# Performance work log

Measured on AMD Instinct MI355X. Metric: run time of the kernel, lower is better.

The kernel has to match this reference:

```python
import jax, jax.numpy as jnp
import numpy as np

B, BOUNDS, NRIM, K, UNITS = 4096, 512, 6, 4, 600
H_IN, DK_IN, DV_IN = 4, 64, 400
H_C, DK_C, DV_C = 4, 32, 100


def setup_inputs() -> dict:
    key = jax.random.key(0)
    ks = jax.random.split(key, 16)
    s = 0.02
    return {
        'inputs': jax.random.normal(ks[0], (B, BOUNDS + NRIM), jnp.float32),
        'hs': jax.random.normal(ks[1], (B, NRIM, UNITS), jnp.float32) * s,
        'cs': jax.random.normal(ks[2], (B, NRIM, UNITS), jnp.float32) * s,
        'Wk': jax.random.normal(ks[3], (BOUNDS, H_IN * DK_IN), jnp.float32) * s,
        'bk': jnp.zeros((H_IN * DK_IN,), jnp.float32),
        'Wv': jax.random.normal(ks[4], (BOUNDS, H_IN * DV_IN), jnp.float32) * s,
        'bv': jnp.zeros((H_IN * DV_IN,), jnp.float32),
        'Wq': jax.random.normal(ks[5], (NRIM, UNITS, H_IN * DK_IN), jnp.float32) * s,
        'lstm_k': jax.random.normal(ks[6], (NRIM, DV_IN, 4 * UNITS), jnp.float32) * s,
        'lstm_r': jax.random.normal(ks[7], (NRIM, UNITS, 4 * UNITS), jnp.float32) * s,
        'lstm_b': jnp.zeros((NRIM, 4 * UNITS), jnp.float32),
        'Wkc': jax.random.normal(ks[8], (NRIM, UNITS, H_C * DK_C), jnp.float32) * s,
        'Wvc': jax.random.normal(ks[9], (NRIM, UNITS, H_C * DV_C), jnp.float32) * s,
        'Wqc': jax.random.normal(ks[10], (NRIM, UNITS, H_C * DK_C), jnp.float32) * s,
        'Wout': jax.random.normal(ks[11], (NRIM, H_C * DV_C, UNITS), jnp.float32) * s,
    }


def _split_heads(t, n_heads, d_head):
    # [B, T, n_heads*d_head] -> [B, n_heads, T, d_head] (matches tf.split+stack)
    b, t_len = t.shape[0], t.shape[1]
    return t.reshape(b, t_len, n_heads, d_head).transpose(0, 2, 1, 3)


def reference(inputs, hs, cs, Wk, bk, Wv, bv, Wq, lstm_k, lstm_r, lstm_b, Wkc, Wvc, Wqc, Wout):
    x = inputs[:, :BOUNDS]                                   # [B, bounds]
    rim_dist = inputs[:, BOUNDS:BOUNDS + NRIM]               # [B, nRIM]

    # ---- input attention ----
    xx = jnp.stack([x, jnp.zeros_like(x)], axis=1)           # [B, 2, bounds]
    k_lay = xx @ Wk + bk                                     # [B, 2, H*dk]
    v_lay = xx @ Wv + bv                                     # [B, 2, H*dv]
    q_lay = jnp.einsum('bnu,nuo->bno', hs, Wq)               # grouped linear [B, nRIM, H*dq]
    kh = _split_heads(k_lay, H_IN, DK_IN)                    # [B, H, 2, dk]
    vh = _split_heads(v_lay, H_IN, DV_IN)                    # [B, H, 2, dv]
    qh = _split_heads(q_lay, H_IN, DK_IN)                    # [B, H, nRIM, dk]
    v2 = vh.mean(axis=1)                                     # [B, 2, dv]
    scores = jnp.einsum('bhnd,bhtd->bhnt', qh, kh) / np.sqrt(DK_IN).astype(np.float32)
    scores2 = scores.mean(axis=1)                            # [B, nRIM, 2]

    # top-k RIM selection mask from RIM_dist (use_attn=False path)
    _, idx = jax.lax.top_k(rim_dist, K)                      # [B, K]
    mask = jnp.zeros((inputs.shape[0], NRIM), inputs.dtype)
    mask = mask.at[jnp.arange(inputs.shape[0])[:, None], idx].set(1.0)[..., None]  # [B, nRIM, 1]

    probs = jax.nn.softmax(scores2, axis=-1)                 # dropout inactive (training=False)
    rnn_in = jnp.einsum('bnt,btv->bnv', probs, v2) * mask    # [B, nRIM, dv]

    # ---- grouped LSTM (keras gate order i,f,c,o) ----
    gates = (jnp.einsum('bnv,nvo->bno', rnn_in, lstm_k)
             + jnp.einsum('bnu,nuo->bno', hs, lstm_r) + lstm_b)  # [B, nRIM, 4*units]
    i, f, g, o = jnp.split(gates, 4, axis=-1)
    c_rnn = jax.nn.sigmoid(f) * cs + jax.nn.sigmoid(i) * jnp.tanh(g)
    h_rnn = jax.nn.sigmoid(o) * jnp.tanh(c_rnn)
    h_new = jax.lax.stop_gradient(h_rnn * (1.0 - mask)) + h_rnn * mask

    # ---- communication attention among RIMs ----
    kc = _split_heads(jnp.einsum('bnu,nuo->bno', h_new, Wkc), H_C, DK_C)  # [B, Hc, nRIM, dkc]
    vc = _split_heads(jnp.einsum('bnu,nuo->bno', h_new, Wvc), H_C, DV_C)
    qc = _split_heads(jnp.einsum('bnu,nuo->bno', h_new, Wqc), H_C, DK_C)
    sc = jnp.einsum('bhnd,bhmd->bhnm', qc, kc) / np.sqrt(DK_C).astype(np.float32)
    pc = jax.nn.softmax(sc, axis=-1) * mask[:, None, :, :]   # zero rows of inactive query RIMs
    ctx = jnp.einsum('bhnm,bhmv->bhnv', pc, vc)              # [B, Hc, nRIM, dvc]
    ctx = ctx.transpose(0, 2, 1, 3).reshape(inputs.shape[0], NRIM, H_C * DV_C)
    h_comm = jnp.einsum('bno,nou->bnu', ctx, Wout) + h_new   # grouped output proj + residual

    # ---- masked state update ----
    h_upd = h_comm * mask + hs * (1.0 - mask)
    c_upd = c_rnn * mask + cs * (1.0 - mask)
    out_state = h_upd.reshape(inputs.shape[0], UNITS * NRIM)
    return out_state, h_upd, c_upd
```

## Files before the change

### kernel.cpp

```cpp
#include <hip/hip_runtime.h>

namespace {
typedef unsigned short u16;
typedef __attribute__((ext_vector_type(8))) __bf16 bf16x8;
typedef __attribute__((ext_vector_type(4))) float f32x4;

constexpr long long kB  = 4096;
constexpr long long kOS = kB * 3600;
constexpr size_t kGAs = 4096ull * 1088;
constexpr int kHnS = 3648;

constexpr size_t oWkvT  = 0;
constexpr size_t oWqT   = oWkvT  + 768ull*512*2;
constexpr size_t oWcomT = oWqT   + 6ull*256*640*2;
constexpr size_t oWoutT = oWcomT + 6ull*768*640*2;
constexpr size_t oLstmT = oWoutT + 6ull*640*448*2;
constexpr size_t oBp    = oLstmT + 6ull*2560*1024*2;
constexpr size_t oBkv   = oBp    + 6ull*2560*4;
constexpr size_t oMask  = oBkv   + 768*4;
constexpr size_t oArena = oMask  + 4096ull*6*4;
constexpr size_t oGA    = oArena;
constexpr size_t oKV    = oGA   + 6ull*kGAs*2;
constexpr size_t oXbf   = oKV   + 4096ull*768*2;
constexpr size_t oQlay  = oXbf;
constexpr size_t oCqv   = oArena;
constexpr size_t oCtx   = oCqv  + 4096ull*4608*2;
}

__device__ __forceinline__ u16 f2b(float f) {
  union { float f; unsigned u; } x; x.f = f;
  unsigned r = (x.u + 0x7fffu + ((x.u >> 16) & 1u)) >> 16;
  return (u16)r;
}
__device__ __forceinline__ float b2f(u16 u) {
  union { unsigned u; float f; } x; x.u = ((unsigned)u) << 16;
  return x.f;
}
__device__ __forceinline__ float sigmoidf_(float x) { return 1.f / (1.f + __expf(-x)); }
__device__ __forceinline__ float tanhf_(float x) {
  const float e = __expf(2.f * x);
  return 1.f - 2.f / (e + 1.f);
}

__device__ __forceinline__ void gload16(const void* g, void* l) {
  __builtin_amdgcn_global_load_lds((const __attribute__((address_space(1))) void*)g,
                                   (__attribute__((address_space(3))) void*)l, 16, 0, 0);
}

union FragU4 { uint4 u4; bf16x8 v; };

template<int MODE>
__global__ __launch_bounds__(256, 2) void gemm64(
    const u16* __restrict__ A, int lda, long strideA,
    const u16* __restrict__ Bt, long strideB, int Kpad,
    void* __restrict__ C, int ldc, int strideC,
    const float* __restrict__ bias, int strideBias,
    int N, int nks, int storeBf16, int nx,
    const float* __restrict__ mask, float* __restrict__ h_upd,
    const float* __restrict__ hs_in, float* __restrict__ out_state)
{
  __shared__ __align__(16) u16 lds[2 * 16384];

  const int nwg = gridDim.x;
  const int orig = blockIdx.x;
  int wgid;
  {
    const int q = nwg >> 3, r = nwg & 7;
    const int xcd = orig & 7, bidx = orig >> 3;
    wgid = (xcd < r ? xcd * (q + 1) : r * (q + 1) + (xcd - r) * q) + bidx;
  }
  const int xt = wgid % nx;
  const int t2 = wgid / nx;
  const int mt = t2 & 31;
  const int rim = t2 >> 5;
  const int m0 = mt * 128, n0 = xt * 128;

  A += (size_t)rim * strideA;
  Bt += (size_t)rim * strideB;
  if (bias) bias += (size_t)rim * strideBias;

  const int t = threadIdx.x;
  const int w = t >> 6, lane = t & 63;
  const int lrow = lane & 15, lk = lane >> 4;
  const int wr = w >> 1, wc = w & 1;

  f32x4 acc[4][4] = {};

  const u16* aS[4]; const u16* bS[4]; int cC[4];
#pragma unroll
  for (int i = 0; i < 4; ++i) {
    const int c = t + i * 256;
    const int row = c >> 3, slot = c & 7;
    cC[i] = c;
    aS[i] = A  + (size_t)(m0 + row) * lda  + ((slot ^ (row & 7)) << 3);
    bS[i] = Bt + (size_t)(n0 + row) * Kpad + ((slot ^ (row & 7)) << 3);
  }
  auto stage = [&](u16* dst) {
#pragma unroll
    for (int i = 0; i < 4; ++i) gload16(aS[i], dst + (size_t)cC[i] * 8);
#pragma unroll
    for (int i = 0; i < 4; ++i) gload16(bS[i], dst + 8192 + (size_t)cC[i] * 8);
#pragma unroll
    for (int i = 0; i < 4; ++i) { aS[i] += 64; bS[i] += 64; }
  };

  stage(lds);
  asm volatile("s_waitcnt vmcnt(0)" ::: "memory");
  __builtin_amdgcn_s_barrier();

  for (int s = 0; s < nks; ++s) {
    const bool more = (s + 1 < nks);
    if (more) stage(lds + ((s + 1) & 1) * 16384);
    __builtin_amdgcn_sched_barrier(0);
    const char* Ab = (const char*)(lds + (s & 1) * 16384);
    const char* Bb = Ab + 16384;
#pragma unroll
    for (int ks = 0; ks < 2; ++ks) {
      FragU4 af[4], bf4[4];
#pragma unroll
      for (int mf = 0; mf < 4; ++mf) {
        const int rr = wr * 64 + mf * 16 + lrow;
        af[mf].u4 = *(const uint4*)(Ab + rr * 128 + ((((ks << 2) | lk) ^ (rr & 7)) << 4));
      }
#pragma unroll
      for (int nf = 0; nf < 4; ++nf) {
        const int rr = wc * 64 + nf * 16 + lrow;
        bf4[nf].u4 = *(const uint4*)(Bb + rr * 128 + ((((ks << 2) | lk) ^ (rr & 7)) << 4));
      }
#pragma unroll
      for (int mf = 0; mf < 4; ++mf)
#pragma unroll
        for (int nf = 0; nf < 4; ++nf)
          acc[mf][nf] = __builtin_amdgcn_mfma_f32_16x16x32_bf16(af[mf].v, bf4[nf].v, acc[mf][nf], 0, 0, 0);
    }
    if (more) {
      asm volatile("s_waitcnt vmcnt(0)" ::: "memory");
      __builtin_amdgcn_s_barrier();
    }
  }

  if (MODE == 0) {
    float* Cf = (float*)C + (size_t)rim * strideC;
    u16*   Cu = (u16*)C + (size_t)rim * strideC;
#pragma unroll
    for (int mf = 0; mf < 4; ++mf)
#pragma unroll
      for (int r2 = 0; r2 < 4; ++r2) {
        const int m = m0 + wr * 64 + mf * 16 + 4 * lk + r2;
#pragma unroll
        for (int nf = 0; nf < 4; ++nf) {
          const int col = n0 + wc * 64 + nf * 16 + lrow;
          if (col < N) {
            float v = acc[mf][nf][r2];
            if (bias) v += bias[col];
            const size_t off = (size_t)m * ldc + col;
            if (storeBf16) Cu[off] = f2b(v); else Cf[off] = v;
          }
        }
      }
  } else {
#pragma unroll
    for (int mf = 0; mf < 4; ++mf)
#pragma unroll
      for (int r2 = 0; r2 < 4; ++r2) {
        const int m = m0 + wr * 64 + mf * 16 + 4 * lk + r2;
        const float mk = mask[(size_t)m * 6 + rim];
#pragma unroll
        for (int nf = 0; nf < 4; ++nf) {
          const int col = n0 + wc * 64 + nf * 16 + lrow;
          if (col < 600) {
            const size_t off = (size_t)m * 3600 + rim * 600 + col;
            const float v = (mk != 0.f) ? (acc[mf][nf][r2] + h_upd[off]) : hs_in[off];
            h_upd[off] = v;
            out_state[off] = v;
          }
        }
      }
  }
}

__global__ __launch_bounds__(512, 2) void gates256(
    const u16* __restrict__ A, const u16* __restrict__ Bt,
    const float* __restrict__ bp, const float* __restrict__ cs,
    const float* __restrict__ mask,
    float* __restrict__ c_upd, float* __restrict__ h_upd, u16* __restrict__ hnbf)
{
  __shared__ __align__(16) u16 lds[2 * 32768];

  const int orig = blockIdx.x;
  const int wgid = (orig & 7) * 120 + (orig >> 3);
  const int rim = wgid / 160;
  const int rem = wgid % 160;
  const int half = rem / 80;
  const int r2d = rem % 80;
  const int mt = r2d / 5;
  const int xt = half * 5 + r2d % 5;
  const int m0 = mt * 256, n0 = xt * 256;

  const u16* Ar = A + (size_t)rim * kGAs;
  const u16* Br = Bt + (size_t)rim * (2560ull * 1024);
  const float* bip = bp + (size_t)rim * 2560;

  const int t = threadIdx.x;
  const int w = t >> 6, lane = t & 63;
  const int lrow = lane & 15, lk = lane >> 4;
  const int wr = w >> 2, wc = w & 3;

  f32x4 acc[8][4] = {};

  const u16* aS[4]; const u16* bS[4]; int cC[4];
#pragma unroll
  for (int i = 0; i < 4; ++i) {
    const int c = t + i * 512;
    const int row = c >> 3, slot = c & 7;
    cC[i] = c;
    aS[i] = Ar + (size_t)(m0 + row) * 1088 + ((slot ^ (row & 7)) << 3);
    bS[i] = Br + (size_t)(n0 + row) * 1024 + ((slot ^ (row & 7)) << 3);
  }
  auto stage = [&](u16* dst) {
#pragma unroll
    for (int i = 0; i < 4; ++i) gload16(aS[i], dst + (size_t)cC[i] * 8);
#pragma unroll
    for (int i = 0; i < 4; ++i) gload16(bS[i], dst + 16384 + (size_t)cC[i] * 8);
#pragma unroll
    for (int i = 0; i < 4; ++i) { aS[i] += 64; bS[i] += 64; }
  };

  constexpr int nks = 16;
  stage(lds);
  asm volatile("s_waitcnt vmcnt(0)" ::: "memory");
  __builtin_amdgcn_s_barrier();

  for (int s = 0; s < nks; ++s) {
    const bool more = (s + 1 < nks);
    if (more) stage(lds + ((s + 1) & 1) * 32768);
    __builtin_amdgcn_sched_barrier(0);
    const char* Ab = (const char*)(lds + (s & 1) * 32768);
    const char* Bb = Ab + 32768;
#pragma unroll
    for (int ks = 0; ks < 2; ++ks) {
      FragU4 af[8], bf4[4];
#pragma unroll
      for (int mf = 0; mf < 8; ++mf) {
        const int rr = wr * 128 + mf * 16 + lrow;
        af[mf].u4 = *(const uint4*)(Ab + rr * 128 + ((((ks << 2) | lk) ^ (rr & 7)) << 4));
      }
#pragma unroll
      for (int nf = 0; nf < 4; ++nf) {
        const int rr = wc * 64 + nf * 16 + lrow;
        bf4[nf].u4 = *(const uint4*)(Bb + rr * 128 + ((((ks << 2) | lk) ^ (rr & 7)) << 4));
      }
#pragma unroll
      for (int mf = 0; mf < 8; ++mf)
#pragma unroll
        for (int nf = 0; nf < 4; ++nf)
          acc[mf][nf] = __builtin_amdgcn_mfma_f32_16x16x32_bf16(af[mf].v, bf4[nf].v, acc[mf][nf], 0, 0, 0);
    }
    if (more) {
      asm volatile("s_waitcnt vmcnt(0)" ::: "memory");
      __builtin_amdgcn_s_barrier();
    }
  }

  const int nb = n0 + wc * 64;
  const int u = ((nb >> 6) << 4) + lrow;
  if (u < 600) {
    const float b_i = bip[nb + lrow];
    const float b_f = bip[nb + 16 + lrow];
    const float b_g = bip[nb + 32 + lrow];
    const float b_o = bip[nb + 48 + lrow];
#pragma unroll
    for (int mf = 0; mf < 8; ++mf)
#pragma unroll
      for (int r2 = 0; r2 < 4; ++r2) {
        const int m = m0 + wr * 128 + mf * 16 + 4 * lk + r2;
        const float iv = acc[mf][0][r2] + b_i;
        const float fv = acc[mf][1][r2] + b_f;
        const float gv = acc[mf][2][r2] + b_g;
        const float ov = acc[mf][3][r2] + b_o;
        const size_t off = (size_t)m * 3600 + rim * 600 + u;
        const float cprev = cs[off];
        const float cv = sigmoidf_(fv) * cprev + sigmoidf_(iv) * tanhf_(gv);
        const float hv = sigmoidf_(ov) * tanhf_(cv);
        const float mk = mask[(size_t)m * 6 + rim];
        c_upd[off] = (mk != 0.f) ? cv : cprev;
        h_upd[off] = hv;
        hnbf[(size_t)m * kHnS + rim * 600 + u] = f2b(hv);
      }
  }
}

__device__ void pack_wt_body(float (*tile)[65], int bx, int by, int rim,
    const float* __restrict__ i1, long s1, const float* __restrict__ i2, long s2,
    int K1, int Ktot, int ldin, int Nreal,
    u16* __restrict__ out, long so, int Kpad, int gateperm, int tid)
{
  i1 += (size_t)rim * s1;
  if (i2) i2 += (size_t)rim * s2;
  u16* o = out + (size_t)rim * so;
  const int n0 = bx * 64, k0 = by * 64;
  const int lane = tid & 63, qq = tid >> 6;
  const int n = n0 + lane;
  int col;
  if (gateperm) {
    const int g = (n >> 4) & 3, u = ((n >> 6) << 4) + (n & 15);
    col = (u < 600) ? g * 600 + u : -1;
  } else {
    col = (n < Nreal) ? n : -1;
  }
#pragma unroll
  for (int i = 0; i < 16; ++i) {
    const int kk = qq + 4 * i;
    const int k = k0 + kk;
    float v = 0.f;
    if (col >= 0) {
      if (k < K1) v = i1[(size_t)k * ldin + col];
      else if (k < Ktot) v = i2[(size_t)(k - K1) * ldin + col];
    }
    tile[kk][lane] = v;
  }
  __syncthreads();
#pragma unroll
  for (int i = 0; i < 16; ++i) {
    const int nn = qq + 4 * i;
    const int k = k0 + lane;
    if (k < Kpad) o[(size_t)(n0 + nn) * Kpad + k] = f2b(tile[lane][nn]);
  }
}

__global__ __launch_bounds__(256) void megapack_w(
    const float* __restrict__ Wk, const float* __restrict__ Wv,
    const float* __restrict__ Wkc, const float* __restrict__ Wqc, const float* __restrict__ Wvc,
    const float* __restrict__ Wq, const float* __restrict__ Wout,
    const float* __restrict__ lstm_k, const float* __restrict__ lstm_r,
    u16* __restrict__ WkvT, u16* __restrict__ WcomT, u16* __restrict__ WqT,
    u16* __restrict__ WoutT, u16* __restrict__ LstmT)
{
  __shared__ float tile[64][65];
  const int id = blockIdx.x, t = threadIdx.x;
  if (id < 3840) {
    const int bx = id % 40, by = (id / 40) % 16, bz = id / 640;
    pack_wt_body(tile, bx, by, bz, lstm_k, 400l*2400, lstm_r, 600l*2400,
                 400, 1000, 2400, 2400, LstmT, 2560l*1024, 1024, 1, t);
  } else if (id < 4260) {
    const int i2 = id - 3840;
    const int bx = i2 % 10, by = (i2 / 10) % 7, bz = i2 / 70;
    pack_wt_body(tile, bx, by, bz, Wout, 400l*600, nullptr, 0,
                 400, 400, 600, 600, WoutT, 640l*448, 448, 0, t);
  } else if (id < 4500) {
    const int i3 = id - 4260;
    const int bx = i3 % 4, by = (i3 / 4) % 10, bz = i3 / 40;
    pack_wt_body(tile, bx, by, bz, Wq, 600l*256, nullptr, 0,
                 600, 600, 256, 256, WqT, 256l*640, 640, 0, t);
  } else if (id < 4692) {
    const int e8 = ((id - 4500) * 256 + t) * 8;
    const int n = e8 >> 9, k0 = e8 & 511;
    u16 st[8];
#pragma unroll
    for (int j = 0; j < 8; ++j) {
      const int k = k0 + j;
      float v = 0.f;
      if (n < 256) v = Wk[(size_t)k * 256 + n];
      else if (n < 656) {
        const float* p = Wv + (size_t)k * 1600 + (n - 256);
        v = 0.25f * (p[0] + p[400] + p[800] + p[1200]);
      }
      st[j] = f2b(v);
    }
    *(uint4*)(WkvT + e8) = *(const uint4*)st;
  } else {
    const long long e8 = ((long long)(id - 4692) * 256 + t) * 8;
    const int rim = (int)(e8 / 491520);
    const int rem = (int)(e8 % 491520);
    const int n = rem / 640, k0 = rem % 640;
    u16 st[8];
#pragma unroll
    for (int j = 0; j < 8; ++j) {
      const int k = k0 + j;
      float v = 0.f;
      if (k < 600) {
        if (n < 128)      v = Wkc[(size_t)rim * 76800 + (size_t)k * 128 + n];
        else if (n < 256) v = Wqc[(size_t)rim * 76800 + (size_t)k * 128 + (n - 128)];
        else if (n < 656) v = Wvc[(size_t)rim * 240000 + (size_t)k * 400 + (n - 256)];
      }
      st[j] = f2b(v);
    }
    *(uint4*)(WcomT + e8) = *(const uint4*)st;
  }
}

__global__ __launch_bounds__(256) void megapack_act(
    const float* __restrict__ inputs, const float* __restrict__ hs,
    const float* __restrict__ lstm_b, const float* __restrict__ bk, const float* __restrict__ bv,
    u16* __restrict__ xbf, u16* __restrict__ gA, float* __restrict__ bp, float* __restrict__ bkv,
    u16* __restrict__ hnbf)
{
  __shared__ float row[3600];
  const int id = blockIdx.x, t = threadIdx.x;
  if (id < 4096) {
    const int b = id;
    for (int i = t; i < 3600; i += 256) row[i] = hs[(size_t)b * 3600 + i];
    __syncthreads();
    for (int c = t; c < 516; c += 256) {
      const int rim = c / 86;
      const int j = (c % 86) * 8;
      u16 v[8];
#pragma unroll
      for (int k = 0; k < 8; ++k) {
        const int col = j + k;
        v[k] = (col < 600) ? f2b(row[rim * 600 + col]) : (u16)0;
      }
      *(uint4*)(gA + (size_t)rim * kGAs + (size_t)b * 1088 + 400 + j) = *(const uint4*)v;
    }
    if (t < 6) {
      u16 z[8] = {0,0,0,0,0,0,0,0};
      *(uint4*)(hnbf + (size_t)b * kHnS + 3600 + t * 8) = *(const uint4*)z;
    }
  } else if (id < 5120) {
    const int e8 = ((id - 4096) * 256 + t) * 8;
    const int b = e8 >> 9, c0 = e8 & 511;
    const float* src = inputs + (size_t)b * 518 + c0;
    u16 st[8];
#pragma unroll
    for (int j = 0; j < 8; ++j) st[j] = f2b(src[j]);
    *(uint4*)(xbf + e8) = *(const uint4*)st;
  } else {
    const int tt = (id - 5120) * 256 + t;
    if (tt < 6 * 2560) {
      const int rim = tt / 2560, p = tt % 2560;
      const int g = (p >> 4) & 3, u = ((p >> 6) << 4) + (p & 15);
      bp[tt] = (u < 600) ? lstm_b[(size_t)rim * 2400 + g * 600 + u] : 0.f;
    }
    if (tt < 768) {
      float v = 0.f;
      if (tt < 256) v = bk[tt];
      else if (tt < 656) { const int j2 = tt - 256; v = 0.25f * (bv[j2] + bv[j2+400] + bv[j2+800] + bv[j2+1200]); }
      bkv[tt] = v;
    }
  }
}

__global__ __launch_bounds__(256) void score_kernel(
    const float* __restrict__ inputs, const u16* __restrict__ qlayb,
    const u16* __restrict__ kvb, const float* __restrict__ bk,
    const float* __restrict__ bkv,
    float* __restrict__ maskout, u16* __restrict__ gA)
{
  const int b = blockIdx.x;
  const int t = threadIdx.x;
  __shared__ float red[4][12];
  __shared__ float sprob[12];
  __shared__ float smask[6];

  const float k0v = b2f(kvb[(size_t)b * 768 + t]);
  const float bkv_ = bk[t];
  float part[12];
#pragma unroll
  for (int n = 0; n < 6; ++n) {
    const float q = b2f(qlayb[(size_t)b * 1536 + n * 256 + t]);
    part[2 * n]     = q * k0v;
    part[2 * n + 1] = q * bkv_;
  }
#pragma unroll
  for (int off = 32; off > 0; off >>= 1)
#pragma unroll
    for (int i = 0; i < 12; ++i)
      part[i] += __shfl_down(part[i], off);
  const int wave = t >> 6, lane = t & 63;
  if (lane == 0)
#pragma unroll
    for (int i = 0; i < 12; ++i) red[wave][i] = part[i];
  __syncthreads();
  if (t < 12) red[0][t] = (red[0][t] + red[1][t] + red[2][t] + red[3][t]) * (1.0f / 32.0f);
  __syncthreads();
  if (t < 6) {
    const float s0 = red[0][2 * t], s1 = red[0][2 * t + 1];
    const float mx = fmaxf(s0, s1);
    const float e0 = __expf(s0 - mx), e1 = __expf(s1 - mx);
    const float inv = 1.f / (e0 + e1);
    sprob[2 * t] = e0 * inv;
    sprob[2 * t + 1] = e1 * inv;
    const float* rd = inputs + (size_t)b * 518 + 512;
    const float mine = rd[t];
    int rank = 0;
#pragma unroll
    for (int j = 0; j < 6; ++j) {
      const float o = rd[j];
      rank += (o > mine) || (o == mine && j < t);
    }
    const float mk = (rank < 4) ? 1.f : 0.f;
    smask[t] = mk;
    maskout[(size_t)b * 6 + t] = mk;
  }
  __syncthreads();
  for (int c = t; c < 300; c += 256) {
    const int n = c / 50;
    const int v = (c % 50) * 8;
    const float p0 = sprob[2 * n], p1 = sprob[2 * n + 1], mk = smask[n];
    u16 st[8];
#pragma unroll
    for (int k = 0; k < 8; ++k)
      st[k] = f2b((p0 * b2f(kvb[(size_t)b * 768 + 256 + v + k]) + p1 * bkv[256 + v + k]) * mk);
    *reinterpret_cast<uint4*>(gA + (size_t)n * kGAs + (size_t)b * 1088 + v) =
        *reinterpret_cast<const uint4*>(st);
  }
}

__global__ __launch_bounds__(256) void comm_kernel(
    const u16* __restrict__ cqv, u16* __restrict__ ctx)
{
  const int b = blockIdx.x, t = threadIdx.x;
  __shared__ float skc[768], sqc[768], svc[2400];
  __shared__ float spc[4][6][6];
  for (int i = t * 4; i < 4608; i += 1024) {
    const ushort4 u4 = *reinterpret_cast<const ushort4*>(cqv + (size_t)b * 4608 + i);
    const u16 uu[4] = {u4.x, u4.y, u4.z, u4.w};
#pragma unroll
    for (int j = 0; j < 4; ++j) {
      const int ii = i + j;
      const int m = ii / 768, c = ii % 768;
      const float v = b2f(uu[j]);
      if (c < 128) skc[m * 128 + c] = v;
      else if (c < 256) sqc[m * 128 + (c - 128)] = v;
      else if (c < 656) svc[m * 400 + (c - 256)] = v;
    }
  }
  __syncthreads();
  if (t < 144) {
    const int h = t / 36, n = (t % 36) / 6, m = t % 6;
    float s = 0.f;
#pragma unroll
    for (int d = 0; d < 32; ++d) s += sqc[n * 128 + h * 32 + d] * skc[m * 128 + h * 32 + d];
    spc[h][n][m] = s * 0.17677669529663687f;
  }
  __syncthreads();
  if (t < 24) {
    const int h = t / 6, n = t % 6;
    float mx = -3.0e38f;
#pragma unroll
    for (int m = 0; m < 6; ++m) mx = fmaxf(mx, spc[h][n][m]);
    float e[6], sum = 0.f;
#pragma unroll
    for (int m = 0; m < 6; ++m) { e[m] = __expf(spc[h][n][m] - mx); sum += e[m]; }
    const float inv = 1.f / sum;
#pragma unroll
    for (int m = 0; m < 6; ++m) spc[h][n][m] = e[m] * inv;
  }
  __syncthreads();
  for (int base = t * 4; base < 2400; base += 1024) {
    const int n = base / 400, rr = base % 400, h = rr / 100, v = rr % 100;
    ushort4 st;
    float s0 = 0.f, s1 = 0.f, s2 = 0.f, s3 = 0.f;
#pragma unroll
    for (int m = 0; m < 6; ++m) {
      const float p = spc[h][n][m];
      const float* vm = &svc[m * 400 + h * 100 + v];
      s0 += p * vm[0]; s1 += p * vm[1]; s2 += p * vm[2]; s3 += p * vm[3];
    }
    st.x = f2b(s0); st.y = f2b(s1); st.z = f2b(s2); st.w = f2b(s3);
    *reinterpret_cast<ushort4*>(ctx + (size_t)b * 2400 + base) = st;
  }
}

extern "C" void kernel_launch(void* const* d_in, const int* in_sizes, int n_in,
                              void* d_out, int out_size, void* d_ws, size_t ws_size,
                              hipStream_t stream) {
  const float* inputs = (const float*)d_in[0];
  const float* hs     = (const float*)d_in[1];
  const float* cs     = (const float*)d_in[2];
  const float* Wk     = (const float*)d_in[3];
  const float* bk     = (const float*)d_in[4];
  const float* Wv     = (const float*)d_in[5];
  const float* bv     = (const float*)d_in[6];
  const float* Wq     = (const float*)d_in[7];
  const float* lstm_k = (const float*)d_in[8];
  const float* lstm_r = (const float*)d_in[9];
  const float* lstm_b = (const float*)d_in[10];
  const float* Wkc    = (const float*)d_in[11];
  const float* Wvc    = (const float*)d_in[12];
  const float* Wqc    = (const float*)d_in[13];
  const float* Wout   = (const float*)d_in[14];

  float* out = (float*)d_out;
  float* out_state = out;
  float* h_upd = out + kOS;
  float* c_upd = out + 2 * kOS;
  u16*   hnbf  = (u16*)d_out;

  char* wsb = (char*)d_ws;
  u16* WkvT  = (u16*)(wsb + oWkvT);
  u16* WqT   = (u16*)(wsb + oWqT);
  u16* WcomT = (u16*)(wsb + oWcomT);
  u16* WoutT = (u16*)(wsb + oWoutT);
  u16* LstmT = (u16*)(wsb + oLstmT);
  float* bp    = (float*)(wsb + oBp);
  float* bkv   = (float*)(wsb + oBkv);
  float* maskf = (float*)(wsb + oMask);
  u16* gA    = (u16*)(wsb + oGA);
  u16* kvb   = (u16*)(wsb + oKV);
  u16* xbf   = (u16*)(wsb + oXbf);
  u16* qlayb = (u16*)(wsb + oQlay);
  u16* cqvb  = (u16*)(wsb + oCqv);
  u16* ctxb  = (u16*)(wsb + oCtx);

  dim3 B256(256);

  megapack_w<<<6132, B256, 0, stream>>>(Wk, Wv, Wkc, Wqc, Wvc, Wq, Wout, lstm_k, lstm_r,
                                        WkvT, WcomT, WqT, WoutT, LstmT);
  megapack_act<<<5180, B256, 0, stream>>>(inputs, hs, lstm_b, bk, bv, xbf, gA, bp, bkv, hnbf);

  gemm64<0><<<dim3(192), B256, 0, stream>>>(xbf, 512, 0, WkvT, 0, 512,
      kvb, 768, 0, bkv, 0, 656, 8, 1, 6,
      nullptr, nullptr, nullptr, nullptr);
  gemm64<0><<<dim3(384), B256, 0, stream>>>(gA + 400, 1088, (long)kGAs, WqT, 256l*640, 640,
      qlayb, 1536, 256, nullptr, 0, 256, 10, 1, 2,
      nullptr, nullptr, nullptr, nullptr);

  score_kernel<<<4096, B256, 0, stream>>>(inputs, qlayb, kvb, bk, bkv, maskf, gA);

  gates256<<<dim3(960), dim3(512), 0, stream>>>(gA, LstmT, bp, cs, maskf, c_upd, h_upd, hnbf);

  gemm64<0><<<dim3(1152), B256, 0, stream>>>(hnbf, kHnS, 600, WcomT, 768l*640, 640,
      cqvb, 4608, 768, nullptr, 0, 656, 10, 1, 6,
      nullptr, nullptr, nullptr, nullptr);

  comm_kernel<<<4096, B256, 0, stream>>>(cqvb, ctxb);

  gemm64<1><<<dim3(960), B256, 0, stream>>>(ctxb, 2400, 400, WoutT, 640l*448, 448,
      nullptr, 0, 0, nullptr, 0, 600, 7, 0, 5,
      maskf, h_upd, hs, out_state);
}
```

Measured before the change: 576.2 us.

## Split LSTM GEMM K-tile into halves with finer-grained prefetch and new LDS swizzle

Restructures the main LSTM gate GEMM mainloop so each 64-wide K tile is staged as two 32-wide halves per operand. Global loads for the next tile are interleaved between MFMA groups, and partial vmcnt waits replace full drains. The LDS layout changes to pack two rows per 128-byte line with a new XOR swizzle, and s_setprio raises wave priority around MFMA bursts. The aim is to overlap memory traffic with matrix math and cut barrier stalls, at the cost of more barriers per tile and more complex indexing that could hurt correctness or occupancy.

```diff
diff --git a/kernel.cpp b/kernel.cpp
--- a/kernel.cpp
+++ b/kernel.cpp
@@ -208,58 +208,112 @@
 
   f32x4 acc[8][4] = {};
 
-  const u16* aS[4]; const u16* bS[4]; int cC[4];
-#pragma unroll
-  for (int i = 0; i < 4; ++i) {
+  const u16* aP[2]; const u16* bP[2]; int dC[2];
+#pragma unroll
+  for (int i = 0; i < 2; ++i) {
     const int c = t + i * 512;
-    const int row = c >> 3, slot = c & 7;
-    cC[i] = c;
-    aS[i] = Ar + (size_t)(m0 + row) * 1088 + ((slot ^ (row & 7)) << 3);
-    bS[i] = Br + (size_t)(n0 + row) * 1024 + ((slot ^ (row & 7)) << 3);
-  }
-  auto stage = [&](u16* dst) {
-#pragma unroll
-    for (int i = 0; i < 4; ++i) gload16(aS[i], dst + (size_t)cC[i] * 8);
-#pragma unroll
-    for (int i = 0; i < 4; ++i) gload16(bS[i], dst + 16384 + (size_t)cC[i] * 8);
-#pragma unroll
-    for (int i = 0; i < 4; ++i) { aS[i] += 64; bS[i] += 64; }
+    const int grow = 2 * (c >> 3) + ((c >> 2) & 1);
+    const int su2 = (c & 3) ^ ((c >> 3) & 3);
+    dC[i] = c * 8;
+    aP[i] = Ar + (size_t)(m0 + grow) * 1088 + su2 * 8;
+    bP[i] = Br + (size_t)(n0 + grow) * 1024 + su2 * 8;
+  }
+  auto stageU = [&](int isB, int kh, int ktile, u16* buf) {
+    u16* dst = buf + (isB ? 16384 : 0) + kh * 8192;
+    const int go = ktile * 64 + kh * 32;
+#pragma unroll
+    for (int i = 0; i < 2; ++i)
+      gload16((isB ? bP[i] : aP[i]) + go, dst + dC[i]);
   };
 
   constexpr int nks = 16;
-  stage(lds);
-  asm volatile("s_waitcnt vmcnt(0)" ::: "memory");
-  __builtin_amdgcn_s_barrier();
-
-  for (int s = 0; s < nks; ++s) {
-    const bool more = (s + 1 < nks);
-    if (more) stage(lds + ((s + 1) & 1) * 32768);
+  stageU(0, 0, 0, lds); stageU(1, 0, 0, lds); stageU(0, 1, 0, lds); stageU(1, 1, 0, lds);
+
+  for (int T = 0; T < nks; ++T) {
+    const char* tb = (const char*)(lds + (T & 1) * 32768);
+    const char* Ah[2] = { tb, tb + 16384 };
+    const char* Bh[2] = { tb + 32768, tb + 49152 };
+    u16* nxt = lds + ((T + 1) & 1) * 32768;
+    const bool st = (T + 1 < nks);
+
+    FragU4 af[4], bfr[4];
+
+    asm volatile("s_waitcnt vmcnt(4)\ns_barrier" ::: "memory");
     __builtin_amdgcn_sched_barrier(0);
-    const char* Ab = (const char*)(lds + (s & 1) * 32768);
-    const char* Bb = Ab + 32768;
-#pragma unroll
-    for (int ks = 0; ks < 2; ++ks) {
-      FragU4 af[8], bf4[4];
-#pragma unroll
-      for (int mf = 0; mf < 8; ++mf) {
-        const int rr = wr * 128 + mf * 16 + lrow;
-        af[mf].u4 = *(const uint4*)(Ab + rr * 128 + ((((ks << 2) | lk) ^ (rr & 7)) << 4));
-      }
-#pragma unroll
-      for (int nf = 0; nf < 4; ++nf) {
-        const int rr = wc * 64 + nf * 16 + lrow;
-        bf4[nf].u4 = *(const uint4*)(Bb + rr * 128 + ((((ks << 2) | lk) ^ (rr & 7)) << 4));
-      }
-#pragma unroll
-      for (int mf = 0; mf < 8; ++mf)
-#pragma unroll
-        for (int nf = 0; nf < 4; ++nf)
-          acc[mf][nf] = __builtin_amdgcn_mfma_f32_16x16x32_bf16(af[mf].v, bf4[nf].v, acc[mf][nf], 0, 0, 0);
-    }
-    if (more) {
-      asm volatile("s_waitcnt vmcnt(0)" ::: "memory");
-      __builtin_amdgcn_s_barrier();
-    }
+#pragma unroll
+    for (int nf = 0; nf < 4; ++nf) {
+      const int rr = wc * 64 + nf * 16 + lrow;
+      bfr[nf].u4 = *(const uint4*)(Bh[0] + (rr >> 1) * 128 +
+                   ((((rr & 1) << 2) | (lk ^ ((rr >> 1) & 3))) << 4));
+    }
+#pragma unroll
+    for (int mf = 0; mf < 4; ++mf) {
+      const int rr = wr * 128 + mf * 16 + lrow;
+      af[mf].u4 = *(const uint4*)(Ah[0] + (rr >> 1) * 128 +
+                  ((((rr & 1) << 2) | (lk ^ ((rr >> 1) & 3))) << 4));
+    }
+    if (st) stageU(0, 0, T + 1, nxt);
+    __builtin_amdgcn_s_setprio(1);
+#pragma unroll
+    for (int mf = 0; mf < 4; ++mf)
+#pragma unroll
+      for (int nf = 0; nf < 4; ++nf)
+        acc[mf][nf] = __builtin_amdgcn_mfma_f32_16x16x32_bf16(af[mf].v, bfr[nf].v, acc[mf][nf], 0, 0, 0);
+    __builtin_amdgcn_s_setprio(0);
+
+#pragma unroll
+    for (int mf = 0; mf < 4; ++mf) {
+      const int rr = wr * 128 + 64 + mf * 16 + lrow;
+      af[mf].u4 = *(const uint4*)(Ah[0] + (rr >> 1) * 128 +
+                  ((((rr & 1) << 2) | (lk ^ ((rr >> 1) & 3))) << 4));
+    }
+    if (st) stageU(1, 0, T + 1, nxt);
+    __builtin_amdgcn_s_setprio(1);
+#pragma unroll
+    for (int mf = 0; mf < 4; ++mf)
+#pragma unroll
+      for (int nf = 0; nf < 4; ++nf)
+        acc[4 + mf][nf] = __builtin_amdgcn_mfma_f32_16x16x32_bf16(af[mf].v, bfr[nf].v, acc[4 + mf][nf], 0, 0, 0);
+    __builtin_amdgcn_s_setprio(0);
+
+    if (st) asm volatile("s_waitcnt vmcnt(4)\ns_barrier" ::: "memory");
+    else    asm volatile("s_waitcnt vmcnt(0)\ns_barrier" ::: "memory");
+    __builtin_amdgcn_sched_barrier(0);
+#pragma unroll
+    for (int nf = 0; nf < 4; ++nf) {
+      const int rr = wc * 64 + nf * 16 + lrow;
+      bfr[nf].u4 = *(const uint4*)(Bh[1] + (rr >> 1) * 128 +
+                   ((((rr & 1) << 2) | (lk ^ ((rr >> 1) & 3))) << 4));
+    }
+#pragma unroll
+    for (int mf = 0; mf < 4; ++mf) {
+      const int rr = wr * 128 + mf * 16 + lrow;
+      af[mf].u4 = *(const uint4*)(Ah[1] + (rr >> 1) * 128 +
+                  ((((rr & 1) << 2) | (lk ^ ((rr >> 1) & 3))) << 4));
+    }
+    if (st) stageU(0, 1, T + 1, nxt);
+    __builtin_amdgcn_s_setprio(1);
+#pragma unroll
+    for (int mf = 0; mf < 4; ++mf)
+#pragma unroll
+      for (int nf = 0; nf < 4; ++nf)
+        acc[mf][nf] = __builtin_amdgcn_mfma_f32_16x16x32_bf16(af[mf].v, bfr[nf].v, acc[mf][nf], 0, 0, 0);
+    __builtin_amdgcn_s_setprio(0);
+
+#pragma unroll
+    for (int mf = 0; mf < 4; ++mf) {
+      const int rr = wr * 128 + 64 + mf * 16 + lrow;
+      af[mf].u4 = *(const uint4*)(Ah[1] + (rr >> 1) * 128 +
+                  ((((rr & 1) << 2) | (lk ^ ((rr >> 1) & 3))) << 4));
+    }
+    if (st) stageU(1, 1, T + 1, nxt);
+    __builtin_amdgcn_s_setprio(1);
+#pragma unroll
+    for (int mf = 0; mf < 4; ++mf)
+#pragma unroll
+      for (int nf = 0; nf < 4; ++nf)
+        acc[4 + mf][nf] = __builtin_amdgcn_mfma_f32_16x16x32_bf16(af[mf].v, bfr[nf].v, acc[4 + mf][nf], 0, 0, 0);
+    __builtin_amdgcn_s_setprio(0);
   }
 
   const int nb = n0 + wc * 64;
```

After: 563.0 us, median of 3. 2.3% less time.
